# Optimization experiments

Hardware: AMD Instinct MI355X
Metric: run time of the kernel (lower is better)

The kernel has to match this reference:

```python
import jax, jax.numpy as jnp
import numpy as np

SCALE_DTYPE = jnp.float32

def rotate_half(x):
    half = x.shape[-1] // 2
    return jnp.concatenate([-x[..., half:], x[..., :half]], axis=-1)

def apply_rope(x, cos, sin):
    # x: [B,T,H,Dh]; cos/sin: [T,Dh] -> broadcast to [1,T,1,Dh]
    c = cos[None, :, None, :]
    s = sin[None, :, None, :]
    return x * c + rotate_half(x) * s

def setup_inputs() -> dict:
    key = jax.random.key(0)
    ks = jax.random.split(key, 7)
    B, T, D, H, Dh = 4, 2048, 1024, 16, 64
    x = jax.random.normal(ks[0], (B, T, D), dtype=jnp.float32)
    cos = jax.random.uniform(ks[1], (T, Dh), dtype=jnp.float32)
    sin = jax.random.uniform(ks[2], (T, Dh), dtype=jnp.float32)
    scale = 1.0 / np.sqrt(D)
    Wq = jax.random.normal(ks[3], (D, D), dtype=jnp.float32) * scale
    Wk = jax.random.normal(ks[4], (D, D), dtype=jnp.float32) * scale
    Wv = jax.random.normal(ks[5], (D, D), dtype=jnp.float32) * scale
    Wo = jax.random.normal(ks[6], (D, D), dtype=jnp.float32) * scale
    return {"x": x, "cos": cos, "sin": sin, "Wq": Wq, "Wk": Wk, "Wv": Wv, "Wo": Wo}

def reference(x, cos, sin, Wq, Wk, Wv, Wo):
    B, T, D = x.shape
    H, Dh = 16, 64
    # Linear projections (weights stored [in, out]) and split heads
    q = (x @ Wq).reshape(B, T, H, Dh)
    k = (x @ Wk).reshape(B, T, H, Dh)
    v = (x @ Wv).reshape(B, T, H, Dh)
    q = apply_rope(q, cos[:T], sin[:T])
    k = apply_rope(k, cos[:T], sin[:T])
    scale = 1.0 / jnp.sqrt(jnp.asarray(Dh, dtype=x.dtype))
    # [B,H,T,T] causal scores
    scores = jnp.einsum('bthd,bshd->bhts', q, k) * scale
    causal = jnp.tril(jnp.ones((T, T), dtype=bool))
    scores = jnp.where(causal[None, None, :, :], scores, jnp.asarray(-jnp.inf, dtype=scores.dtype))
    weights = jax.nn.softmax(scores, axis=-1)
    out = jnp.einsum('bhts,bshd->bthd', weights, v).reshape(B, T, D)
    return out @ Wo
```

## Files before the change

kernel.cpp:

```cpp
#include <hip/hip_runtime.h>
#include <cstdint>
#include <cstddef>

typedef unsigned short ushort_t;
typedef __attribute__((ext_vector_type(8))) short short8;
typedef __attribute__((ext_vector_type(4))) float float4v;
typedef __attribute__((ext_vector_type(4))) unsigned short ushort4v;

__device__ __forceinline__ float b2f(ushort_t u) {
    uint32_t x = ((uint32_t)u) << 16;
    float f;
    __builtin_memcpy(&f, &x, 4);
    return f;
}
__device__ __forceinline__ ushort_t f2b(float f) {
    uint32_t x;
    __builtin_memcpy(&x, &f, 4);
    uint32_t r = (x + 0x7fffu + ((x >> 16) & 1u)) >> 16;
    return (ushort_t)r;
}
__device__ __forceinline__ ushort_t f2b_trunc(float f) {
    uint32_t x;
    __builtin_memcpy(&x, &f, 4);
    return (ushort_t)(x >> 16);
}

typedef __attribute__((address_space(3))) void lds_void;
typedef __attribute__((address_space(1))) const void gbl_void;
__device__ __forceinline__ void gload16(const void* g, void* l) {
    __builtin_amdgcn_global_load_lds((gbl_void*)(uintptr_t)g, (lds_void*)(uintptr_t)l, 16, 0, 0);
}

__global__ void detect_dtype(const ushort_t* __restrict__ cosp, int* __restrict__ flag) {
    int tid = threadIdx.x;
    int bad = 0;
    for (int i = tid; i < 512; i += 64) {
        ushort_t u = cosp[i];
        int sign = u >> 15;
        int e = (u >> 7) & 0xFF;
        if (sign || e > 126) bad = 1;
    }
    int anybad = __any(bad);
    if (tid == 0) *flag = anybad ? 1 : 0;
}

__global__ __launch_bounds__(256) void convert_x(const void* __restrict__ in,
                                                 ushort_t* __restrict__ out,
                                                 const int* __restrict__ flag) {
    if (*flag == 0) return;
    int i = (blockIdx.x * 256 + threadIdx.x) * 4;
    float4v v = *(const float4v*)((const float*)in + i);
    ushort4v o;
#pragma unroll
    for (int j = 0; j < 4; ++j) o[j] = f2b(v[j]);
    *(ushort4v*)(out + i) = o;
}

__global__ __launch_bounds__(256) void convert_cs(const void* __restrict__ c,
                                                  const void* __restrict__ s,
                                                  ushort_t* __restrict__ cb,
                                                  ushort_t* __restrict__ sb,
                                                  const int* __restrict__ flag) {
    int f = *flag;
    int i = blockIdx.x * 256 + threadIdx.x;
    if (i >= 131072) return;
    if (f) {
        cb[i] = f2b(((const float*)c)[i]);
        sb[i] = f2b(((const float*)s)[i]);
    } else {
        cb[i] = ((const ushort_t*)c)[i];
        sb[i] = ((const ushort_t*)s)[i];
    }
}

__global__ __launch_bounds__(256) void transpose_w4(const void* __restrict__ w0,
                                                    const void* __restrict__ w1,
                                                    const void* __restrict__ w2,
                                                    const void* __restrict__ w3,
                                                    ushort_t* __restrict__ out,
                                                    const int* __restrict__ flag) {
    int f = *flag;
    int z = blockIdx.z;
    const void* in = (z == 0) ? w0 : (z == 1) ? w1 : (z == 2) ? w2 : w3;
    ushort_t* o = out + (size_t)z * 1024 * 1024;
    __shared__ ushort_t tile[32][33];
    int bx = blockIdx.x * 32;
    int by = blockIdx.y * 32;
    int tx = threadIdx.x & 31;
    int ty = threadIdx.x >> 5;
    for (int r = ty; r < 32; r += 8) {
        size_t idx = (size_t)(by + r) * 1024 + bx + tx;
        tile[r][tx] = f ? f2b(((const float*)in)[idx]) : ((const ushort_t*)in)[idx];
    }
    __syncthreads();
    for (int r = ty; r < 32; r += 8)
        o[(size_t)(bx + r) * 1024 + by + tx] = tile[tx][r];
}

__global__ __launch_bounds__(256) void gemm_qkv(const ushort_t* __restrict__ X0,
                                                const ushort_t* __restrict__ X1,
                                                const ushort_t* __restrict__ Wt,
                                                ushort_t* __restrict__ qk,
                                                ushort_t* __restrict__ vt,
                                                const ushort_t* __restrict__ cosb,
                                                const ushort_t* __restrict__ sinb,
                                                const int* __restrict__ flagp) {
    __shared__ ushort_t Al[128 * 64];
    __shared__ ushort_t Bl[128 * 64];

    int tid = threadIdx.x;
    int lane = tid & 63;
    int wave = tid >> 6;
    int wr = wave >> 1;
    int wc = wave & 1;
    int quad = lane >> 4;
    int l16 = lane & 15;

    int id = blockIdx.x;
    int nb = (id & 7) + 8 * ((id >> 3) % 3);
    int mb = id / 24;
    int m0 = mb * 128;
    int n0 = nb * 128;

    const ushort_t* Xb = (*flagp) ? X1 : X0;

    int lrow = lane >> 3;
    int lcol = (lane & 7) * 8;

    float4v acc[4][4];
#pragma unroll
    for (int i = 0; i < 4; ++i)
#pragma unroll
        for (int j = 0; j < 4; ++j) acc[i][j] = (float4v){0.f, 0.f, 0.f, 0.f};

    for (int k0 = 0; k0 < 1024; k0 += 64) {
        __syncthreads();
#pragma unroll
        for (int p = 0; p < 4; ++p) {
            int row = wave * 32 + p * 8 + lrow;
            gload16(Xb + (size_t)(m0 + row) * 1024 + k0 + lcol, &Al[(size_t)(wave * 4 + p) * 512]);
            gload16(Wt + (size_t)(n0 + row) * 1024 + k0 + lcol, &Bl[(size_t)(wave * 4 + p) * 512]);
        }
        __syncthreads();

#pragma unroll
        for (int ks = 0; ks < 2; ++ks) {
            int kf = ks * 32 + quad * 8;
            short8 a_frag[4], b_frag[4];
#pragma unroll
            for (int i = 0; i < 4; ++i) {
                a_frag[i] = *(const short8*)(&Al[(wr * 64 + i * 16 + l16) * 64 + kf]);
                b_frag[i] = *(const short8*)(&Bl[(wc * 64 + i * 16 + l16) * 64 + kf]);
            }
#pragma unroll
            for (int i = 0; i < 4; ++i)
#pragma unroll
                for (int j = 0; j < 4; ++j)
                    acc[i][j] = __builtin_amdgcn_mfma_f32_16x16x32_bf16(
                        a_frag[i], b_frag[j], acc[i][j], 0, 0, 0);
        }
    }

    int nglob = n0 + wc * 64;
    int region = nglob >> 10;
    int hcol = (nglob & 1023) >> 6;

    if (region < 2) {
        int colbase = region * 1024 + hcol * 64 + l16;
#pragma unroll
        for (int i = 0; i < 4; ++i) {
            int rowb = m0 + wr * 64 + i * 16 + quad * 4;
#pragma unroll
            for (int r = 0; r < 4; ++r) {
                int row = rowb + r;
                int t = row & 2047;
                const ushort_t* cp = cosb + t * 64 + l16;
                const ushort_t* sp = sinb + t * 64 + l16;
                float c0 = b2f(cp[0]), c1 = b2f(cp[16]), c2 = b2f(cp[32]), c3 = b2f(cp[48]);
                float s0 = b2f(sp[0]), s1 = b2f(sp[16]), s2 = b2f(sp[32]), s3 = b2f(sp[48]);
                float a0 = acc[i][0][r], a1 = acc[i][1][r], a2 = acc[i][2][r], a3 = acc[i][3][r];
                float o0 = a0 * c0 - a2 * s0;
                float o1 = a1 * c1 - a3 * s1;
                float o2 = a2 * c2 + a0 * s2;
                float o3 = a3 * c3 + a1 * s3;
                size_t base = (size_t)row * 2048 + colbase;
                qk[base] = f2b(o0);
                qk[base + 16] = f2b(o1);
                qk[base + 32] = f2b(o2);
                qk[base + 48] = f2b(o3);
            }
        }
    } else {
#pragma unroll
        for (int i = 0; i < 4; ++i) {
            int rowb = m0 + wr * 64 + i * 16 + quad * 4;
            int b = rowb >> 11;
            int t0 = rowb & 2047;
            size_t hb = (size_t)(b * 16 + hcol) * 64;
#pragma unroll
            for (int j = 0; j < 4; ++j) {
                int d = l16 + j * 16;
                ushort4v pk;
#pragma unroll
                for (int r = 0; r < 4; ++r) pk[r] = f2b(acc[i][j][r]);
                *(ushort4v*)(vt + (hb + d) * 2048 + t0) = pk;
            }
        }
    }
}

__global__ __launch_bounds__(256) void gemm_proj(const ushort_t* __restrict__ A, int lda,
                                                 const ushort_t* __restrict__ Bt,
                                                 void* __restrict__ C, int ldc,
                                                 int K,
                                                 const int* __restrict__ flagp) {
    __shared__ ushort_t Al[128 * 64];
    __shared__ ushort_t Bl[128 * 64];

    int tid = threadIdx.x;
    int lane = tid & 63;
    int wave = tid >> 6;
    int wr = wave >> 1;
    int wc = wave & 1;
    int quad = lane >> 4;
    int l16 = lane & 15;

    int id = blockIdx.x;
    int m0 = (id >> 3) * 128;
    int n0 = (id & 7) * 128;

    int lrow = lane >> 3;
    int lcol = (lane & 7) * 8;

    float4v acc[4][4];
#pragma unroll
    for (int i = 0; i < 4; ++i)
#pragma unroll
        for (int j = 0; j < 4; ++j) acc[i][j] = (float4v){0.f, 0.f, 0.f, 0.f};

    for (int k0 = 0; k0 < K; k0 += 64) {
        __syncthreads();
#pragma unroll
        for (int p = 0; p < 4; ++p) {
            int row = wave * 32 + p * 8 + lrow;
            gload16(A + (size_t)(m0 + row) * lda + k0 + lcol, &Al[(size_t)(wave * 4 + p) * 512]);
            gload16(Bt + (size_t)(n0 + row) * K + k0 + lcol, &Bl[(size_t)(wave * 4 + p) * 512]);
        }
        __syncthreads();

#pragma unroll
        for (int ks = 0; ks < 2; ++ks) {
            int kf = ks * 32 + quad * 8;
            short8 a_frag[4], b_frag[4];
#pragma unroll
            for (int i = 0; i < 4; ++i) {
                a_frag[i] = *(const short8*)(&Al[(wr * 64 + i * 16 + l16) * 64 + kf]);
                b_frag[i] = *(const short8*)(&Bl[(wc * 64 + i * 16 + l16) * 64 + kf]);
            }
#pragma unroll
            for (int i = 0; i < 4; ++i)
#pragma unroll
                for (int j = 0; j < 4; ++j)
                    acc[i][j] = __builtin_amdgcn_mfma_f32_16x16x32_bf16(
                        a_frag[i], b_frag[j], acc[i][j], 0, 0, 0);
        }
    }

    int f32out = *flagp;

#pragma unroll
    for (int i = 0; i < 4; ++i) {
        int rowb = m0 + wr * 64 + i * 16 + quad * 4;
#pragma unroll
        for (int r = 0; r < 4; ++r) {
            size_t base = (size_t)(rowb + r) * ldc + n0 + wc * 64 + l16;
            if (f32out) {
                float* Cf = (float*)C;
#pragma unroll
                for (int j = 0; j < 4; ++j) Cf[base + j * 16] = acc[i][j][r];
            } else {
                ushort_t* Cb = (ushort_t*)C;
#pragma unroll
                for (int j = 0; j < 4; ++j) Cb[base + j * 16] = f2b(acc[i][j][r]);
            }
        }
    }
}

__global__ __launch_bounds__(512, 4) void attn_mfma(ushort_t* qk,
                                                    const ushort_t* __restrict__ vt) {
    __shared__ ushort_t Kl[64 * 72];
    __shared__ ushort_t Vl[64 * 72];
    __shared__ ushort_t Pl[8 * 16 * 72];

    int tid = threadIdx.x;
    int lane = tid & 63;
    int wave = tid >> 6;
    int quad = lane >> 4;
    int l16 = lane & 15;

    int bxi = blockIdx.x;
    int bh = blockIdx.y;
    int b = bh >> 4;
    int h = bh & 15;

    ushort_t* Pw = &Pl[wave * 16 * 72];
    int rr = tid >> 3;
    int cc = (tid & 7) * 8;

    const float SCL = 0.125f * 1.44269504f;
    const float SMAX2 = 20.0f * 1.44269504f;

#pragma unroll 1
    for (int phase = 0; phase < 2; ++phase) {
        int qt = phase ? bxi : (15 - bxi);
        int row0 = qt * 128 + wave * 16;
        size_t qbase = ((size_t)(b * 2048 + row0)) * 2048 + h * 64;

        short8 qf[2];
        {
            const ushort_t* p = qk + qbase + (size_t)l16 * 2048 + quad * 8;
            qf[0] = *(const short8*)p;
            qf[1] = *(const short8*)(p + 32);
        }

        float4v oacc[4];
#pragma unroll
        for (int nt = 0; nt < 4; ++nt) oacc[nt] = (float4v){0.f, 0.f, 0.f, 0.f};
        float psum[4];
#pragma unroll
        for (int r = 0; r < 4; ++r) psum[r] = 0.f;

        int ntiles = 2 * qt + 2;

        short8 kreg, vreg;
        kreg = *(const short8*)(qk + ((size_t)(b * 2048 + rr)) * 2048 + 1024 + h * 64 + cc);
        vreg = *(const short8*)(vt + ((size_t)(bh * 64 + rr)) * 2048 + cc);

        for (int st = 0; st < ntiles; ++st) {
            int s0 = st * 64;
            __syncthreads();
            *(short8*)(&Kl[rr * 72 + cc]) = kreg;
            *(short8*)(&Vl[rr * 72 + cc]) = vreg;
            __syncthreads();

            if (st + 1 < ntiles) {
                int s1 = s0 + 64;
                kreg = *(const short8*)(qk + ((size_t)(b * 2048 + s1 + rr)) * 2048 + 1024 + h * 64 + cc);
                vreg = *(const short8*)(vt + ((size_t)(bh * 64 + rr)) * 2048 + s1 + cc);
            }

            if (s0 <= row0 + 15) {
                float4v sacc[4];
#pragma unroll
                for (int ct = 0; ct < 4; ++ct) sacc[ct] = (float4v){0.f, 0.f, 0.f, 0.f};
#pragma unroll
                for (int ks = 0; ks < 2; ++ks) {
                    short8 bfr[4];
#pragma unroll
                    for (int ct = 0; ct < 4; ++ct)
                        bfr[ct] = *(const short8*)(&Kl[(ct * 16 + l16) * 72 + ks * 32 + quad * 8]);
#pragma unroll
                    for (int ct = 0; ct < 4; ++ct)
                        sacc[ct] = __builtin_amdgcn_mfma_f32_16x16x32_bf16(
                            qf[ks], bfr[ct], sacc[ct], 0, 0, 0);
                }

                if ((s0 + 63) > row0) {
#pragma unroll
                    for (int r = 0; r < 4; ++r) {
                        int trow = row0 + quad * 4 + r;
                        float ps = 0.f;
#pragma unroll
                        for (int ct = 0; ct < 4; ++ct) {
                            float p = exp2f(sacc[ct][r] * SCL - SMAX2);
                            if ((s0 + ct * 16 + l16) > trow) p = 0.f;
                            ps += p;
                            Pw[(quad * 4 + r) * 72 + ct * 16 + l16] = f2b_trunc(p);
                        }
                        psum[r] += ps;
                    }
                } else {
#pragma unroll
                    for (int r = 0; r < 4; ++r) {
                        float ps = 0.f;
#pragma unroll
                        for (int ct = 0; ct < 4; ++ct) {
                            float p = exp2f(sacc[ct][r] * SCL - SMAX2);
                            ps += p;
                            Pw[(quad * 4 + r) * 72 + ct * 16 + l16] = f2b_trunc(p);
                        }
                        psum[r] += ps;
                    }
                }

#pragma unroll
                for (int ks = 0; ks < 2; ++ks) {
                    short8 bfr[4];
#pragma unroll
                    for (int nt = 0; nt < 4; ++nt)
                        bfr[nt] = *(const short8*)(&Vl[(nt * 16 + l16) * 72 + ks * 32 + quad * 8]);
                    short8 af = *(const short8*)(&Pw[l16 * 72 + ks * 32 + quad * 8]);
#pragma unroll
                    for (int nt = 0; nt < 4; ++nt)
                        oacc[nt] = __builtin_amdgcn_mfma_f32_16x16x32_bf16(
                            af, bfr[nt], oacc[nt], 0, 0, 0);
                }
            }
        }

#pragma unroll
        for (int r = 0; r < 4; ++r) {
            float ps = psum[r];
#pragma unroll
            for (int off = 1; off < 16; off <<= 1) ps += __shfl_xor(ps, off);
            float inv = 1.0f / ps;
            size_t base = qbase + (size_t)(quad * 4 + r) * 2048;
#pragma unroll
            for (int nt = 0; nt < 4; ++nt)
                qk[base + nt * 16 + l16] = f2b(oacc[nt][r] * inv);
        }
    }
}

extern "C" void kernel_launch(void* const* d_in, const int* in_sizes, int n_in,
                              void* d_out, int out_size, void* d_ws, size_t ws_size,
                              hipStream_t stream) {
    const void* x = d_in[0];
    const void* cosp = d_in[1];
    const void* sinp = d_in[2];
    const void* Wq = d_in[3];
    const void* Wk = d_in[4];
    const void* Wv = d_in[5];
    const void* Wo = d_in[6];

    char* ws = (char*)d_ws;
    int* flag = (int*)ws;
    ushort_t* vtg = (ushort_t*)(ws + 256);
    ushort_t* qk = vtg + (size_t)8192 * 2048;
    ushort_t* WT = qk + (size_t)8192 * 2048;
    ushort_t* WoT = WT + (size_t)3 * 1024 * 1024;
    ushort_t* cosb = WT + (size_t)4 * 1024 * 1024;
    ushort_t* sinb = cosb + (size_t)2048 * 64;
    ushort_t* xb = sinb + (size_t)2048 * 64;

    detect_dtype<<<1, 64, 0, stream>>>((const ushort_t*)cosp, flag);
    convert_cs<<<512, 256, 0, stream>>>(cosp, sinp, cosb, sinb, flag);
    convert_x<<<8192, 256, 0, stream>>>(x, xb, flag);
    transpose_w4<<<dim3(32, 32, 4), 256, 0, stream>>>(Wq, Wk, Wv, Wo, WT, flag);

    gemm_qkv<<<1536, 256, 0, stream>>>((const ushort_t*)x, xb, WT, qk, vtg, cosb, sinb, flag);

    attn_mfma<<<dim3(8, 64), 512, 0, stream>>>(qk, vtg);

    gemm_proj<<<512, 256, 0, stream>>>(qk, 2048, WoT, d_out, 1024, 1024, flag);
}
```

Measured before the change: 293.3 us.

## Rewrite QKV GEMM with 256x256 tiles, swizzled LDS and multi-stage async prefetch

Replaces the QKV projection GEMM's 128x128 single-buffered tile loop with 256x256 tiles per 512-thread block. Global-to-LDS loads run as a multi-stage pipeline using explicit vmcnt waits, with XOR-swizzled LDS layout, raised MFMA priority and sched barriers. The goal is to hide global load latency behind MFMA work and improve data reuse per block. The cost is 128KB of LDS and a larger accumulator register footprint, which limits occupancy and makes correctness depend on the hand-coded wait counts.

```diff
diff --git a/kernel.cpp b/kernel.cpp
--- a/kernel.cpp
+++ b/kernel.cpp
@@ -97,69 +97,161 @@
         o[(size_t)(bx + r) * 1024 + by + tx] = tile[tx][r];
 }
 
-__global__ __launch_bounds__(256) void gemm_qkv(const ushort_t* __restrict__ X0,
-                                                const ushort_t* __restrict__ X1,
-                                                const ushort_t* __restrict__ Wt,
-                                                ushort_t* __restrict__ qk,
-                                                ushort_t* __restrict__ vt,
-                                                const ushort_t* __restrict__ cosb,
-                                                const ushort_t* __restrict__ sinb,
-                                                const int* __restrict__ flagp) {
-    __shared__ ushort_t Al[128 * 64];
-    __shared__ ushort_t Bl[128 * 64];
+struct QkvCtx {
+    char* LDSc;
+    const ushort_t *Asrc0, *Asrc1, *Bsrc0, *Bsrc1;
+    int aoff, boff;
+    int ldsA0, ldsA1, ldsB0, ldsB1;
+};
+
+template <int W>
+__device__ __forceinline__ void wait_vm() {
+    if constexpr (W == 8)      asm volatile("s_waitcnt vmcnt(8)" ::: "memory");
+    else if constexpr (W == 6) asm volatile("s_waitcnt vmcnt(6)" ::: "memory");
+    else if constexpr (W == 4) asm volatile("s_waitcnt vmcnt(4)" ::: "memory");
+    else                       asm volatile("s_waitcnt vmcnt(0)" ::: "memory");
+}
+
+#define QKV_MFMA_QUAD(MH)                                                            \
+    do {                                                                             \
+        __builtin_amdgcn_s_barrier();                                                \
+        asm volatile("s_waitcnt lgkmcnt(0)" ::: "memory");                           \
+        __builtin_amdgcn_sched_barrier(0);                                           \
+        __builtin_amdgcn_s_setprio(1);                                               \
+        _Pragma("unroll") for (int i = 0; i < 4; ++i)                                \
+            _Pragma("unroll") for (int n = 0; n < 4; ++n)                            \
+                acc[(MH)*4 + i][n] = __builtin_amdgcn_mfma_f32_16x16x32_bf16(        \
+                    areg[i], breg[n], acc[(MH)*4 + i][n], 0, 0, 0);                  \
+        __builtin_amdgcn_s_setprio(0);                                               \
+        __builtin_amdgcn_sched_barrier(0);                                           \
+        __builtin_amdgcn_s_barrier();                                                \
+        asm volatile("" ::: "memory");                                               \
+    } while (0)
+
+template <int W1, int W3, bool DO12, bool DO34>
+__device__ __forceinline__ void qkv_ktile(const QkvCtx& C, int p, int jj,
+                                          float4v (&acc)[8][4]) {
+    short8 areg[4], breg[4];
+    const int s0 = (2 * p) * 16384;
+    const int s1 = (2 * p + 1) * 16384;
+
+#pragma unroll
+    for (int n = 0; n < 4; ++n) breg[n] = *(const short8*)(C.LDSc + s0 + C.boff + n * 1024);
+#pragma unroll
+    for (int i = 0; i < 4; ++i) areg[i] = *(const short8*)(C.LDSc + s0 + C.aoff + i * 1024);
+    if (DO12) {
+        int koff = (jj + 1) * 64 + 32;
+        int sl = (2 * (1 - p) + 1) * 16384;
+        gload16(C.Asrc0 + koff, C.LDSc + C.ldsA0 + sl);
+        gload16(C.Asrc1 + koff, C.LDSc + C.ldsA1 + sl);
+    }
+    wait_vm<W1>();
+    QKV_MFMA_QUAD(0);
+
+#pragma unroll
+    for (int i = 0; i < 4; ++i) areg[i] = *(const short8*)(C.LDSc + s0 + C.aoff + 4096 + i * 1024);
+    if (DO12) {
+        int koff = (jj + 1) * 64 + 32;
+        int sl = (2 * (1 - p) + 1) * 16384;
+        gload16(C.Bsrc0 + koff, C.LDSc + C.ldsB0 + sl);
+        gload16(C.Bsrc1 + koff, C.LDSc + C.ldsB1 + sl);
+    }
+    QKV_MFMA_QUAD(1);
+
+#pragma unroll
+    for (int n = 0; n < 4; ++n) breg[n] = *(const short8*)(C.LDSc + s1 + C.boff + n * 1024);
+#pragma unroll
+    for (int i = 0; i < 4; ++i) areg[i] = *(const short8*)(C.LDSc + s1 + C.aoff + i * 1024);
+    if (DO34) {
+        int koff = (jj + 2) * 64;
+        int sl = (2 * p) * 16384;
+        gload16(C.Asrc0 + koff, C.LDSc + C.ldsA0 + sl);
+        gload16(C.Asrc1 + koff, C.LDSc + C.ldsA1 + sl);
+    }
+    wait_vm<W3>();
+    QKV_MFMA_QUAD(0);
+
+#pragma unroll
+    for (int i = 0; i < 4; ++i) areg[i] = *(const short8*)(C.LDSc + s1 + C.aoff + 4096 + i * 1024);
+    if (DO34) {
+        int koff = (jj + 2) * 64;
+        int sl = (2 * p) * 16384;
+        gload16(C.Bsrc0 + koff, C.LDSc + C.ldsB0 + sl);
+        gload16(C.Bsrc1 + koff, C.LDSc + C.ldsB1 + sl);
+    }
+    QKV_MFMA_QUAD(1);
+}
+
+__global__ __launch_bounds__(512, 2) void gemm_qkv(const ushort_t* __restrict__ X0,
+                                                   const ushort_t* __restrict__ X1,
+                                                   const ushort_t* __restrict__ Wt,
+                                                   ushort_t* __restrict__ qk,
+                                                   ushort_t* __restrict__ vt,
+                                                   const ushort_t* __restrict__ cosb,
+                                                   const ushort_t* __restrict__ sinb,
+                                                   const int* __restrict__ flagp) {
+    __shared__ ushort_t LDS[65536];
 
     int tid = threadIdx.x;
     int lane = tid & 63;
     int wave = tid >> 6;
-    int wr = wave >> 1;
-    int wc = wave & 1;
+    int wr = wave >> 2;
+    int wc = wave & 3;
     int quad = lane >> 4;
     int l16 = lane & 15;
 
     int id = blockIdx.x;
-    int nb = (id & 7) + 8 * ((id >> 3) % 3);
-    int mb = id / 24;
-    int m0 = mb * 128;
-    int n0 = nb * 128;
+    int swzid = (id & 7) * 48 + (id >> 3);
+    int m0 = (swzid & 31) * 256;
+    int n0 = (swzid >> 5) * 256;
 
     const ushort_t* Xb = (*flagp) ? X1 : X0;
 
-    int lrow = lane >> 3;
-    int lcol = (lane & 7) * 8;
-
-    float4v acc[4][4];
-#pragma unroll
-    for (int i = 0; i < 4; ++i)
-#pragma unroll
-        for (int j = 0; j < 4; ++j) acc[i][j] = (float4v){0.f, 0.f, 0.f, 0.f};
-
-    for (int k0 = 0; k0 < 1024; k0 += 64) {
-        __syncthreads();
-#pragma unroll
-        for (int p = 0; p < 4; ++p) {
-            int row = wave * 32 + p * 8 + lrow;
-            gload16(Xb + (size_t)(m0 + row) * 1024 + k0 + lcol, &Al[(size_t)(wave * 4 + p) * 512]);
-            gload16(Wt + (size_t)(n0 + row) * 1024 + k0 + lcol, &Bl[(size_t)(wave * 4 + p) * 512]);
-        }
-        __syncthreads();
-
-#pragma unroll
-        for (int ks = 0; ks < 2; ++ks) {
-            int kf = ks * 32 + quad * 8;
-            short8 a_frag[4], b_frag[4];
-#pragma unroll
-            for (int i = 0; i < 4; ++i) {
-                a_frag[i] = *(const short8*)(&Al[(wr * 64 + i * 16 + l16) * 64 + kf]);
-                b_frag[i] = *(const short8*)(&Bl[(wc * 64 + i * 16 + l16) * 64 + kf]);
-            }
-#pragma unroll
-            for (int i = 0; i < 4; ++i)
-#pragma unroll
-                for (int j = 0; j < 4; ++j)
-                    acc[i][j] = __builtin_amdgcn_mfma_f32_16x16x32_bf16(
-                        a_frag[i], b_frag[j], acc[i][j], 0, 0, 0);
-        }
-    }
+    int srow = lane >> 2;
+    int sslot = (lane & 3) ^ ((lane >> 3) & 3);
+    QkvCtx C;
+    C.LDSc = (char*)LDS;
+    C.Asrc0 = Xb + (size_t)(m0 + (wave * 2 + 0) * 16 + srow) * 1024 + sslot * 8;
+    C.Asrc1 = Xb + (size_t)(m0 + (wave * 2 + 1) * 16 + srow) * 1024 + sslot * 8;
+    C.Bsrc0 = Wt + (size_t)(n0 + (wave * 2 + 0) * 16 + srow) * 1024 + sslot * 8;
+    C.Bsrc1 = Wt + (size_t)(n0 + (wave * 2 + 1) * 16 + srow) * 1024 + sslot * 8;
+    C.ldsA0 = (wave * 2 + 0) * 1024;
+    C.ldsA1 = (wave * 2 + 1) * 1024;
+    C.ldsB0 = 65536 + (wave * 2 + 0) * 1024;
+    C.ldsB1 = 65536 + (wave * 2 + 1) * 1024;
+    int swzb = (quad ^ ((l16 >> 1) & 3)) * 16;
+    C.aoff = (wr * 128 + l16) * 64 + swzb;
+    C.boff = 65536 + (wc * 64 + l16) * 64 + swzb;
+
+    float4v acc[8][4];
+#pragma unroll
+    for (int i = 0; i < 8; ++i)
+#pragma unroll
+        for (int n = 0; n < 4; ++n) acc[i][n] = (float4v){0.f, 0.f, 0.f, 0.f};
+
+    gload16(C.Asrc0 + 0, C.LDSc + C.ldsA0 + 0 * 16384);
+    gload16(C.Asrc1 + 0, C.LDSc + C.ldsA1 + 0 * 16384);
+    gload16(C.Bsrc0 + 0, C.LDSc + C.ldsB0 + 0 * 16384);
+    gload16(C.Bsrc1 + 0, C.LDSc + C.ldsB1 + 0 * 16384);
+    gload16(C.Asrc0 + 32, C.LDSc + C.ldsA0 + 1 * 16384);
+    gload16(C.Asrc1 + 32, C.LDSc + C.ldsA1 + 1 * 16384);
+    gload16(C.Bsrc0 + 32, C.LDSc + C.ldsB0 + 1 * 16384);
+    gload16(C.Bsrc1 + 32, C.LDSc + C.ldsB1 + 1 * 16384);
+    gload16(C.Asrc0 + 64, C.LDSc + C.ldsA0 + 2 * 16384);
+    gload16(C.Asrc1 + 64, C.LDSc + C.ldsA1 + 2 * 16384);
+    gload16(C.Bsrc0 + 64, C.LDSc + C.ldsB0 + 2 * 16384);
+    gload16(C.Bsrc1 + 64, C.LDSc + C.ldsB1 + 2 * 16384);
+    wait_vm<8>();
+    __builtin_amdgcn_s_barrier();
+    asm volatile("" ::: "memory");
+
+#pragma unroll 1
+    for (int j = 0; j < 14; j += 2) {
+        qkv_ktile<6, 6, true, true>(C, 0, j, acc);
+        qkv_ktile<6, 6, true, true>(C, 1, j + 1, acc);
+    }
+    qkv_ktile<6, 4, true, false>(C, 0, 14, acc);
+    qkv_ktile<0, 0, false, false>(C, 1, 15, acc);
 
     int nglob = n0 + wc * 64;
     int region = nglob >> 10;
@@ -168,8 +260,8 @@
     if (region < 2) {
         int colbase = region * 1024 + hcol * 64 + l16;
 #pragma unroll
-        for (int i = 0; i < 4; ++i) {
-            int rowb = m0 + wr * 64 + i * 16 + quad * 4;
+        for (int m = 0; m < 8; ++m) {
+            int rowb = m0 + wr * 128 + m * 16 + quad * 4;
 #pragma unroll
             for (int r = 0; r < 4; ++r) {
                 int row = rowb + r;
@@ -177,12 +269,12 @@
                 const ushort_t* cp = cosb + t * 64 + l16;
                 const ushort_t* sp = sinb + t * 64 + l16;
                 float c0 = b2f(cp[0]), c1 = b2f(cp[16]), c2 = b2f(cp[32]), c3 = b2f(cp[48]);
-                float s0 = b2f(sp[0]), s1 = b2f(sp[16]), s2 = b2f(sp[32]), s3 = b2f(sp[48]);
-                float a0 = acc[i][0][r], a1 = acc[i][1][r], a2 = acc[i][2][r], a3 = acc[i][3][r];
-                float o0 = a0 * c0 - a2 * s0;
-                float o1 = a1 * c1 - a3 * s1;
-                float o2 = a2 * c2 + a0 * s2;
-                float o3 = a3 * c3 + a1 * s3;
+                float s0v = b2f(sp[0]), s1v = b2f(sp[16]), s2v = b2f(sp[32]), s3v = b2f(sp[48]);
+                float a0 = acc[m][0][r], a1 = acc[m][1][r], a2 = acc[m][2][r], a3 = acc[m][3][r];
+                float o0 = a0 * c0 - a2 * s0v;
+                float o1 = a1 * c1 - a3 * s1v;
+                float o2 = a2 * c2 + a0 * s2v;
+                float o3 = a3 * c3 + a1 * s3v;
                 size_t base = (size_t)row * 2048 + colbase;
                 qk[base] = f2b(o0);
                 qk[base + 16] = f2b(o1);
@@ -192,17 +284,17 @@
         }
     } else {
 #pragma unroll
-        for (int i = 0; i < 4; ++i) {
-            int rowb = m0 + wr * 64 + i * 16 + quad * 4;
+        for (int m = 0; m < 8; ++m) {
+            int rowb = m0 + wr * 128 + m * 16 + quad * 4;
             int b = rowb >> 11;
             int t0 = rowb & 2047;
             size_t hb = (size_t)(b * 16 + hcol) * 64;
 #pragma unroll
-            for (int j = 0; j < 4; ++j) {
-                int d = l16 + j * 16;
+            for (int n = 0; n < 4; ++n) {
+                int d = l16 + n * 16;
                 ushort4v pk;
 #pragma unroll
-                for (int r = 0; r < 4; ++r) pk[r] = f2b(acc[i][j][r]);
+                for (int r = 0; r < 4; ++r) pk[r] = f2b(acc[m][n][r]);
                 *(ushort4v*)(vt + (hb + d) * 2048 + t0) = pk;
             }
         }
@@ -449,7 +541,7 @@
     convert_x<<<8192, 256, 0, stream>>>(x, xb, flag);
     transpose_w4<<<dim3(32, 32, 4), 256, 0, stream>>>(Wq, Wk, Wv, Wo, WT, flag);
 
-    gemm_qkv<<<1536, 256, 0, stream>>>((const ushort_t*)x, xb, WT, qk, vtg, cosb, sinb, flag);
+    gemm_qkv<<<384, 512, 0, stream>>>((const ushort_t*)x, xb, WT, qk, vtg, cosb, sinb, flag);
 
     attn_mfma<<<dim3(8, 64), 512, 0, stream>>>(qk, vtg);
 
```

Result: faster. 273.7 us (-6.7%).

## Pipeline QKV GEMM with triple-buffered swizzled LDS and 256x128 tiles

Applied to the files above, without the earlier changes.

Rewrites the fused QKV projection GEMM to use 512-thread blocks computing 256x128 tiles. The K loop becomes a three-stage software pipeline in which async global-to-LDS loads run ahead of compute, using a partial vmcnt wait and a single barrier per step. LDS rows are XOR-swizzled to avoid bank conflicts, the block-to-XCD mapping is changed, and MFMA sections are wrapped in s_setprio. The goal is to hide load latency and cut barrier overhead. In exchange it uses much more LDS, which caps occupancy, and the hand-unrolled schedule is fragile.

```diff
diff --git a/kernel.cpp b/kernel.cpp
--- a/kernel.cpp
+++ b/kernel.cpp
@@ -97,71 +97,140 @@
         o[(size_t)(bx + r) * 1024 + by + tx] = tile[tx][r];
 }
 
-__global__ __launch_bounds__(256) void gemm_qkv(const ushort_t* __restrict__ X0,
-                                                const ushort_t* __restrict__ X1,
-                                                const ushort_t* __restrict__ Wt,
-                                                ushort_t* __restrict__ qk,
-                                                ushort_t* __restrict__ vt,
-                                                const ushort_t* __restrict__ cosb,
-                                                const ushort_t* __restrict__ sinb,
-                                                const int* __restrict__ flagp) {
-    __shared__ ushort_t Al[128 * 64];
-    __shared__ ushort_t Bl[128 * 64];
+template <int W>
+__device__ __forceinline__ void vm_wait() {
+    if constexpr (W == 6)      asm volatile("s_waitcnt vmcnt(6)" ::: "memory");
+    else                       asm volatile("s_waitcnt vmcnt(0)" ::: "memory");
+}
+#define KBAR()                                       \
+    do {                                             \
+        asm volatile("" ::: "memory");               \
+        __builtin_amdgcn_s_barrier();                \
+        asm volatile("" ::: "memory");               \
+    } while (0)
+
+__global__ __launch_bounds__(512, 2) void gemm_qkv(const ushort_t* __restrict__ X0,
+                                                   const ushort_t* __restrict__ X1,
+                                                   const ushort_t* __restrict__ Wt,
+                                                   ushort_t* __restrict__ qk,
+                                                   ushort_t* __restrict__ vt,
+                                                   const ushort_t* __restrict__ cosb,
+                                                   const ushort_t* __restrict__ sinb,
+                                                   const int* __restrict__ flagp) {
+    __shared__ ushort_t LDS[73728];
+    char* LDSc = (char*)LDS;
 
     int tid = threadIdx.x;
     int lane = tid & 63;
     int wave = tid >> 6;
-    int wr = wave >> 1;
-    int wc = wave & 1;
+    int wm = wave >> 1;
+    int wn = wave & 1;
     int quad = lane >> 4;
     int l16 = lane & 15;
 
     int id = blockIdx.x;
-    int nb = (id & 7) + 8 * ((id >> 3) % 3);
-    int mb = id / 24;
-    int m0 = mb * 128;
-    int n0 = nb * 128;
+    int xcd = id & 7;
+    int r = id >> 3;
+    int m0 = (r & 31) * 256;
+    int n0 = (xcd * 3 + (r >> 5)) * 128;
 
     const ushort_t* Xb = (*flagp) ? X1 : X0;
 
     int lrow = lane >> 3;
-    int lcol = (lane & 7) * 8;
+    int lslot = (lane & 7) ^ lrow;
+    const ushort_t* aSrc = Xb + (size_t)(m0 + wave * 32 + lrow) * 1024 + lslot * 8;
+    const ushort_t* bSrc = Wt + (size_t)(n0 + wave * 16 + lrow) * 1024 + lslot * 8;
+    int ldsA_w = (wave * 32) * 128;
+    int ldsB_w = (wave * 16) * 128;
+
+    int aoff0 = (wm * 64 + l16) * 128 + ((quad ^ (l16 & 7)) * 16);
+    int aoff1 = (wm * 64 + l16) * 128 + (((4 + quad) ^ (l16 & 7)) * 16);
+    int boff0 = (wn * 64 + l16) * 128 + ((quad ^ (l16 & 7)) * 16);
+    int boff1 = (wn * 64 + l16) * 128 + (((4 + quad) ^ (l16 & 7)) * 16);
 
     float4v acc[4][4];
 #pragma unroll
     for (int i = 0; i < 4; ++i)
 #pragma unroll
-        for (int j = 0; j < 4; ++j) acc[i][j] = (float4v){0.f, 0.f, 0.f, 0.f};
-
-    for (int k0 = 0; k0 < 1024; k0 += 64) {
-        __syncthreads();
-#pragma unroll
-        for (int p = 0; p < 4; ++p) {
-            int row = wave * 32 + p * 8 + lrow;
-            gload16(Xb + (size_t)(m0 + row) * 1024 + k0 + lcol, &Al[(size_t)(wave * 4 + p) * 512]);
-            gload16(Wt + (size_t)(n0 + row) * 1024 + k0 + lcol, &Bl[(size_t)(wave * 4 + p) * 512]);
-        }
-        __syncthreads();
-
-#pragma unroll
-        for (int ks = 0; ks < 2; ++ks) {
-            int kf = ks * 32 + quad * 8;
-            short8 a_frag[4], b_frag[4];
-#pragma unroll
-            for (int i = 0; i < 4; ++i) {
-                a_frag[i] = *(const short8*)(&Al[(wr * 64 + i * 16 + l16) * 64 + kf]);
-                b_frag[i] = *(const short8*)(&Bl[(wc * 64 + i * 16 + l16) * 64 + kf]);
-            }
-#pragma unroll
-            for (int i = 0; i < 4; ++i)
-#pragma unroll
-                for (int j = 0; j < 4; ++j)
-                    acc[i][j] = __builtin_amdgcn_mfma_f32_16x16x32_bf16(
-                        a_frag[i], b_frag[j], acc[i][j], 0, 0, 0);
-        }
-    }
-
-    int nglob = n0 + wc * 64;
+        for (int n = 0; n < 4; ++n) acc[i][n] = (float4v){0.f, 0.f, 0.f, 0.f};
+
+#define STAGE6(t, jj)                                                       \
+    do {                                                                    \
+        const ushort_t* as_ = aSrc + (jj) * 64;                             \
+        const ushort_t* bs_ = bSrc + (jj) * 64;                             \
+        char* al_ = LDSc + (t) * 32768 + ldsA_w;                            \
+        char* bl_ = LDSc + 98304 + (t) * 16384 + ldsB_w;                    \
+        gload16(as_, al_);                                                  \
+        gload16(as_ + 8 * 1024, al_ + 1024);                                \
+        gload16(as_ + 16 * 1024, al_ + 2048);                               \
+        gload16(as_ + 24 * 1024, al_ + 3072);                               \
+        gload16(bs_, bl_);                                                  \
+        gload16(bs_ + 8 * 1024, bl_ + 1024);                                \
+    } while (0)
+
+#define COMPUTE(t)                                                          \
+    do {                                                                    \
+        const char* ab_ = LDSc + (t) * 32768;                               \
+        const char* bb_ = LDSc + 98304 + (t) * 16384;                       \
+        short8 a0_[4], b0_[4], a1_[4], b1_[4];                              \
+        _Pragma("unroll") for (int i = 0; i < 4; ++i) {                     \
+            a0_[i] = *(const short8*)(ab_ + aoff0 + i * 2048);              \
+            a1_[i] = *(const short8*)(ab_ + aoff1 + i * 2048);              \
+        }                                                                   \
+        _Pragma("unroll") for (int n = 0; n < 4; ++n) {                     \
+            b0_[n] = *(const short8*)(bb_ + boff0 + n * 2048);              \
+            b1_[n] = *(const short8*)(bb_ + boff1 + n * 2048);              \
+        }                                                                   \
+        __builtin_amdgcn_s_setprio(1);                                      \
+        _Pragma("unroll") for (int i = 0; i < 4; ++i)                       \
+            _Pragma("unroll") for (int n = 0; n < 4; ++n)                   \
+                acc[i][n] = __builtin_amdgcn_mfma_f32_16x16x32_bf16(        \
+                    a0_[i], b0_[n], acc[i][n], 0, 0, 0);                    \
+        _Pragma("unroll") for (int i = 0; i < 4; ++i)                       \
+            _Pragma("unroll") for (int n = 0; n < 4; ++n)                   \
+                acc[i][n] = __builtin_amdgcn_mfma_f32_16x16x32_bf16(        \
+                    a1_[i], b1_[n], acc[i][n], 0, 0, 0);                    \
+        __builtin_amdgcn_s_setprio(0);                                      \
+    } while (0)
+
+    STAGE6(0, 0);
+    STAGE6(1, 1);
+    vm_wait<6>();
+    KBAR();
+
+#pragma unroll 1
+    for (int g = 0; g < 4; ++g) {
+        int j = g * 3;
+        STAGE6(2, j + 2);
+        COMPUTE(0);
+        vm_wait<6>();
+        KBAR();
+        STAGE6(0, j + 3);
+        COMPUTE(1);
+        vm_wait<6>();
+        KBAR();
+        STAGE6(1, j + 4);
+        COMPUTE(2);
+        vm_wait<6>();
+        KBAR();
+    }
+    STAGE6(2, 14);
+    COMPUTE(0);
+    vm_wait<6>();
+    KBAR();
+    STAGE6(0, 15);
+    COMPUTE(1);
+    vm_wait<6>();
+    KBAR();
+    COMPUTE(2);
+    vm_wait<0>();
+    KBAR();
+    COMPUTE(0);
+
+#undef STAGE6
+#undef COMPUTE
+
+    int nglob = n0 + wn * 64;
     int region = nglob >> 10;
     int hcol = (nglob & 1023) >> 6;
 
@@ -169,20 +238,20 @@
         int colbase = region * 1024 + hcol * 64 + l16;
 #pragma unroll
         for (int i = 0; i < 4; ++i) {
-            int rowb = m0 + wr * 64 + i * 16 + quad * 4;
-#pragma unroll
-            for (int r = 0; r < 4; ++r) {
-                int row = rowb + r;
+            int rowb = m0 + wm * 64 + i * 16 + quad * 4;
+#pragma unroll
+            for (int rr = 0; rr < 4; ++rr) {
+                int row = rowb + rr;
                 int t = row & 2047;
                 const ushort_t* cp = cosb + t * 64 + l16;
                 const ushort_t* sp = sinb + t * 64 + l16;
                 float c0 = b2f(cp[0]), c1 = b2f(cp[16]), c2 = b2f(cp[32]), c3 = b2f(cp[48]);
-                float s0 = b2f(sp[0]), s1 = b2f(sp[16]), s2 = b2f(sp[32]), s3 = b2f(sp[48]);
-                float a0 = acc[i][0][r], a1 = acc[i][1][r], a2 = acc[i][2][r], a3 = acc[i][3][r];
-                float o0 = a0 * c0 - a2 * s0;
-                float o1 = a1 * c1 - a3 * s1;
-                float o2 = a2 * c2 + a0 * s2;
-                float o3 = a3 * c3 + a1 * s3;
+                float s0v = b2f(sp[0]), s1v = b2f(sp[16]), s2v = b2f(sp[32]), s3v = b2f(sp[48]);
+                float a0 = acc[i][0][rr], a1 = acc[i][1][rr], a2 = acc[i][2][rr], a3 = acc[i][3][rr];
+                float o0 = a0 * c0 - a2 * s0v;
+                float o1 = a1 * c1 - a3 * s1v;
+                float o2 = a2 * c2 + a0 * s2v;
+                float o3 = a3 * c3 + a1 * s3v;
                 size_t base = (size_t)row * 2048 + colbase;
                 qk[base] = f2b(o0);
                 qk[base + 16] = f2b(o1);
@@ -193,16 +262,16 @@
     } else {
 #pragma unroll
         for (int i = 0; i < 4; ++i) {
-            int rowb = m0 + wr * 64 + i * 16 + quad * 4;
+            int rowb = m0 + wm * 64 + i * 16 + quad * 4;
             int b = rowb >> 11;
             int t0 = rowb & 2047;
             size_t hb = (size_t)(b * 16 + hcol) * 64;
 #pragma unroll
-            for (int j = 0; j < 4; ++j) {
-                int d = l16 + j * 16;
+            for (int n = 0; n < 4; ++n) {
+                int d = l16 + n * 16;
                 ushort4v pk;
 #pragma unroll
-                for (int r = 0; r < 4; ++r) pk[r] = f2b(acc[i][j][r]);
+                for (int rr = 0; rr < 4; ++rr) pk[rr] = f2b(acc[i][n][rr]);
                 *(ushort4v*)(vt + (hb + d) * 2048 + t0) = pk;
             }
         }
@@ -449,7 +518,7 @@
     convert_x<<<8192, 256, 0, stream>>>(x, xb, flag);
     transpose_w4<<<dim3(32, 32, 4), 256, 0, stream>>>(Wq, Wk, Wv, Wo, WT, flag);
 
-    gemm_qkv<<<1536, 256, 0, stream>>>((const ushort_t*)x, xb, WT, qk, vtg, cosb, sinb, flag);
+    gemm_qkv<<<768, 512, 0, stream>>>((const ushort_t*)x, xb, WT, qk, vtg, cosb, sinb, flag);
 
     attn_mfma<<<dim3(8, 64), 512, 0, stream>>>(qk, vtg);
 
```

Measured after the change: 291.3 us. Within noise of the previous version (-0.7%).
